# Performance work log

Hardware: AMD Instinct MI355X
Metric: run time of the kernel (lower is better)

The kernel has to match this reference:

```python
import jax, jax.numpy as jnp
import numpy as np

N_NODES = 50000
N_EDGES = 800000
HIDDEN = 128
OUT = 128


def setup_inputs() -> dict:
    key = jax.random.key(0)
    k1, k2, k3, k4, k5, k6 = jax.random.split(key, 6)
    h = jax.random.normal(k1, (N_NODES, HIDDEN), dtype=jnp.float32)
    src = jax.random.randint(k2, (N_EDGES,), 0, N_NODES, dtype=jnp.int64)
    dst = jax.random.randint(k3, (N_EDGES,), 0, N_NODES, dtype=jnp.int64)
    scale = 1.0 / np.sqrt(HIDDEN)
    W_edge = jax.random.normal(k4, (OUT, HIDDEN), dtype=jnp.float32) * scale
    W_self = jax.random.normal(k5, (OUT, HIDDEN), dtype=jnp.float32) * scale
    b_self = jax.random.normal(k6, (OUT,), dtype=jnp.float32) * scale
    return {"h": h, "src": src, "dst": dst, "W_edge": W_edge, "W_self": W_self, "b_self": b_self}


def reference(h, src, dst, W_edge, W_self, b_self):
    n = h.shape[0]
    # edge_transform(src_features): same linear on every edge -> transform nodes once, then gather
    msg_node = h @ W_edge.T                       # [N, OUT]
    msg = msg_node[src]                           # [E, OUT] gather
    sums = jax.ops.segment_sum(msg, dst, num_segments=n)  # [N, OUT] scatter-add
    deg = jax.ops.segment_sum(jnp.ones((dst.shape[0],), dtype=h.dtype), dst, num_segments=n)
    h1 = sums / jnp.maximum(deg, 1.0)[:, None]    # mean; zero in-degree -> 0 (DGL semantics)
    out = jax.nn.relu(h @ W_self.T + b_self + h1)
    return out
```

## Files before the change

kernel.cpp:

```cpp
#include <hip/hip_runtime.h>

#define N_HID 128
#define CAP   32
#define OVF_CAP 8192
#define NSLICE 8
#define PBLK   256

typedef short bf16x8 __attribute__((ext_vector_type(8)));
typedef float f32x4  __attribute__((ext_vector_type(4)));

static __device__ __forceinline__ unsigned short f2bf(float f)
{
    unsigned int u = __float_as_uint(f);
    u = (u + 0x7fffu + ((u >> 16) & 1u)) >> 16;
    return (unsigned short)u;
}
static __device__ __forceinline__ unsigned int pack2(float a, float b)
{
    return (unsigned int)f2bf(a) | ((unsigned int)f2bf(b) << 16);
}
static __device__ __forceinline__ float lo_f(unsigned int x)
{
    return __uint_as_float(x << 16);
}
static __device__ __forceinline__ float hi_f(unsigned int x)
{
    return __uint_as_float(x & 0xffff0000u);
}
static __device__ __forceinline__ int slice_of(int d, float sln)
{
    int sl = (int)((float)d * sln);
    return sl > NSLICE - 1 ? NSLICE - 1 : sl;
}

__global__ __launch_bounds__(256) void count_fragw_cast(
    const int* __restrict__ dst, int* __restrict__ blockCnt,
    int* __restrict__ cnt, int* __restrict__ ovfn, int E, int n, float sln,
    const float* __restrict__ We, const float* __restrict__ Ws,
    unsigned short* __restrict__ Be, unsigned short* __restrict__ Bs,
    const float* __restrict__ h, unsigned short* __restrict__ hbf, int total,
    unsigned int* __restrict__ bucket32, unsigned int sent2)
{
    int t = threadIdx.x, b = blockIdx.x;

    if (b >= PBLK + 16) {
        int idx = (b - PBLK - 16) * 2048 + t * 8;
        if (idx + 8 <= total) {
            float4 v0 = *(const float4*)&h[idx];
            float4 v1 = *(const float4*)&h[idx + 4];
            uint4 pk;
            pk.x = pack2(v0.x, v0.y);
            pk.y = pack2(v0.z, v0.w);
            pk.z = pack2(v1.x, v1.y);
            pk.w = pack2(v1.z, v1.w);
            *(uint4*)&hbf[idx] = pk;
        } else if (idx + 8 <= total + N_HID) {
            uint4 z = {0u, 0u, 0u, 0u};
            *(uint4*)&hbf[idx] = z;
        }
        return;
    }

    if (b >= PBLK) {
        int bb = b - PBLK;
        const float* srcw = (bb < 8) ? We : Ws;
        unsigned short* dstF = (bb < 8) ? Be : Bs;
        int rt = bb & 7;
        int kc = t >> 6, l = t & 63, m = l & 15, q = l >> 4;
        const float* p = &srcw[(size_t)(rt * 16 + m) * N_HID + kc * 32 + q * 8];
        float4 v0 = *(const float4*)p;
        float4 v1 = *(const float4*)(p + 4);
        uint4 pk;
        pk.x = pack2(v0.x, v0.y);
        pk.y = pack2(v0.z, v0.w);
        pk.z = pack2(v1.x, v1.y);
        pk.w = pack2(v1.z, v1.w);
        *(uint4*)&dstF[(size_t)rt * 2048 + kc * 512 + l * 8] = pk;
        return;
    }

    for (int i = b * 256 + t; i < n; i += PBLK * 256) cnt[i] = 0;
    {
        const int nb32 = n * (CAP / 2);
        for (int i = b * 256 + t; i < nb32; i += PBLK * 256) bucket32[i] = sent2;
    }
    if (b == 0 && t == 0) *ovfn = 0;

    int c[NSLICE];
#pragma unroll
    for (int s = 0; s < NSLICE; ++s) c[s] = 0;

    for (int e = b * 256 + t; e < E; e += PBLK * 256) {
        int sl = slice_of(dst[e], sln);
#pragma unroll
        for (int s = 0; s < NSLICE; ++s) c[s] += (sl == s);
    }

    __shared__ int red[NSLICE * 4];
    int lane = t & 63, wid = t >> 6;
#pragma unroll
    for (int s = 0; s < NSLICE; ++s) {
        int v = c[s];
#pragma unroll
        for (int off = 32; off; off >>= 1) v += __shfl_down(v, off);
        if (lane == 0) red[s * 4 + wid] = v;
    }
    __syncthreads();
    if (t < NSLICE)
        blockCnt[t * PBLK + b] = red[t*4+0] + red[t*4+1] + red[t*4+2] + red[t*4+3];
}

__global__ __launch_bounds__(256) void part_scan(
    const int* __restrict__ blockCnt, int* __restrict__ blockBase,
    int* __restrict__ sbase, int E)
{
    __shared__ int wsm[4];
    int t = threadIdx.x, lane = t & 63, wid = t >> 6;
    int v[8]; int s = 0;
#pragma unroll
    for (int i = 0; i < 8; ++i) { v[i] = blockCnt[t * 8 + i]; s += v[i]; }
    int val = s;
#pragma unroll
    for (int off = 1; off < 64; off <<= 1) {
        int y = __shfl_up(val, off);
        if (lane >= off) val += y;
    }
    if (lane == 63) wsm[wid] = val;
    __syncthreads();
    if (t == 0) { int a = 0; for (int w = 0; w < 4; ++w) { int tmp = wsm[w]; wsm[w] = a; a += tmp; } }
    __syncthreads();
    int excl = wsm[wid] + val - s;
#pragma unroll
    for (int i = 0; i < 8; ++i) { int tv = v[i]; blockBase[t * 8 + i] = excl; excl += tv; }
    __syncthreads();
    if (t < NSLICE) sbase[t] = blockBase[t * PBLK];
    if (t == 0)     sbase[NSLICE] = E;
}

__global__ __launch_bounds__(256) void part_scatter(
    const int* __restrict__ src, const int* __restrict__ dst,
    const int* __restrict__ blockBase, unsigned int* __restrict__ part,
    int E, int n, float sln)
{
    __shared__ int cur[NSLICE];
    int t = threadIdx.x, b = blockIdx.x;
    if (t < NSLICE) cur[t] = blockBase[t * PBLK + b];
    __syncthreads();
    for (int e = b * 256 + t; e < E; e += PBLK * 256) {
        int d = dst[e], s = src[e];
        int sl  = slice_of(d, sln);
        int pos = atomicAdd(&cur[sl], 1);
        part[pos] = ((unsigned int)d << 16) | (unsigned int)s;
    }
}

__global__ __launch_bounds__(256) void bucket_scatter2(
    const unsigned int* __restrict__ part,
    const int* __restrict__ sbase,
    int* __restrict__ cnt,
    unsigned short* __restrict__ bucket,
    int* __restrict__ ovfn,
    long long* __restrict__ ovf)
{
    const int slice = blockIdx.x & 7;
    const int g     = blockIdx.x >> 3;
    const int nG    = (int)(gridDim.x >> 3);
    const int lo    = sbase[slice];
    const int hi    = sbase[slice + 1];
    const int m     = hi - lo;

    const int chunk = (m + nG - 1) / nG;
    const int e0 = lo + g * chunk;
    int e1 = e0 + chunk; if (e1 > hi) e1 = hi;

    for (int e = e0 + (int)threadIdx.x; e < e1; e += 256) {
        unsigned int pk = part[e];
        int d = (int)(pk >> 16);
        int s = (int)(pk & 0xffffu);
        int c = atomicAdd(&cnt[d], 1);
        if (c < CAP) {
            bucket[(size_t)d * CAP + c] = (unsigned short)s;
        } else {
            int o = atomicAdd(ovfn, 1);
            if (o < OVF_CAP) ovf[o] = ((long long)d << 32) | (unsigned int)s;
        }
    }
}

__global__ __launch_bounds__(512) void gather_gemm(
    const int* __restrict__ cnt,
    const unsigned short* __restrict__ bucket,
    const int* __restrict__ ovfn,
    const long long* __restrict__ ovf,
    const unsigned short* __restrict__ hbf,
    const unsigned short* __restrict__ Be,
    const unsigned short* __restrict__ Bsf,
    const float* __restrict__ bias,
    float* __restrict__ out,
    int n, int nrt)
{
    __shared__ __align__(16) unsigned int wl[16 * 68];

    const int t    = threadIdx.x;
    const int wid  = t >> 6;
    const int lane = t & 63;
    const int q    = lane >> 4;
    const int s    = lane & 15;
    const int slice = blockIdx.x & 7;
    const int g     = blockIdx.x >> 3;
    const int tLo = (int)(((long long)slice * nrt) >> 3);
    const int tHi = (int)(((long long)(slice + 1) * nrt) >> 3);
    const int tile = tLo + g;
    if (tile >= tHi) return;

    const uint4* h4 = (const uint4*)hbf;

#pragma unroll
    for (int k = 0; k < 2; ++k) {
        const int mm   = wid * 2 + k;
        const int node = tile * 16 + mm;
        const unsigned short* bk = &bucket[(size_t)node * CAP];
        float a0=0.f,a1=0.f,a2=0.f,a3=0.f,a4=0.f,a5=0.f,a6=0.f,a7=0.f;
        int deg = node < n ? cnt[node] : 0;

        {
            uint4 vr[4];
#pragma unroll
            for (int i = 0; i < 4; ++i) {
                int r = bk[i * 4 + q];
                vr[i] = h4[(size_t)r * 16 + s];
            }
#pragma unroll
            for (int i = 0; i < 4; ++i) {
                a0 += lo_f(vr[i].x); a1 += hi_f(vr[i].x);
                a2 += lo_f(vr[i].y); a3 += hi_f(vr[i].y);
                a4 += lo_f(vr[i].z); a5 += hi_f(vr[i].z);
                a6 += lo_f(vr[i].w); a7 += hi_f(vr[i].w);
            }
        }
        if (deg > 16) {
            uint4 vr[4];
#pragma unroll
            for (int i = 0; i < 4; ++i) {
                int r = bk[16 + i * 4 + q];
                vr[i] = h4[(size_t)r * 16 + s];
            }
#pragma unroll
            for (int i = 0; i < 4; ++i) {
                a0 += lo_f(vr[i].x); a1 += hi_f(vr[i].x);
                a2 += lo_f(vr[i].y); a3 += hi_f(vr[i].y);
                a4 += lo_f(vr[i].z); a5 += hi_f(vr[i].z);
                a6 += lo_f(vr[i].w); a7 += hi_f(vr[i].w);
            }
        }

        if (deg > CAP) {
            int no = *ovfn; if (no > OVF_CAP) no = OVF_CAP;
            unsigned int qm = (q == 0) ? 0xffffffffu : 0u;
            for (int o = 0; o < no; ++o) {
                long long pk = ovf[o];
                if ((int)(pk >> 32) == node) {
                    uint4 v = h4[(size_t)(unsigned int)pk * 16 + s];
                    unsigned int x;
                    x = v.x & qm; a0 += lo_f(x); a1 += hi_f(x);
                    x = v.y & qm; a2 += lo_f(x); a3 += hi_f(x);
                    x = v.z & qm; a4 += lo_f(x); a5 += hi_f(x);
                    x = v.w & qm; a6 += lo_f(x); a7 += hi_f(x);
                }
            }
        }

#pragma unroll
        for (int off = 16; off <= 32; off <<= 1) {
            a0 += __shfl_xor(a0, off); a1 += __shfl_xor(a1, off);
            a2 += __shfl_xor(a2, off); a3 += __shfl_xor(a3, off);
            a4 += __shfl_xor(a4, off); a5 += __shfl_xor(a5, off);
            a6 += __shfl_xor(a6, off); a7 += __shfl_xor(a7, off);
        }

        float sc = deg > 0 ? 1.0f / (float)deg : 0.f;
        if (q == 0) {
            uint4 pk;
            pk.x = pack2(a0 * sc, a1 * sc);
            pk.y = pack2(a2 * sc, a3 * sc);
            pk.z = pack2(a4 * sc, a5 * sc);
            pk.w = pack2(a6 * sc, a7 * sc);
            *(uint4*)&wl[mm * 68 + 4 * s] = pk;
        }
    }
    __syncthreads();

    const int rr = lane & 15, qq = lane >> 4;
    const int row0 = tile * 16;

    bf16x8 ah[4], ag[4];
#pragma unroll
    for (int kc = 0; kc < 4; ++kc) {
        int gr = row0 + rr; if (gr > n - 1) gr = n - 1;
        ah[kc] = *(const bf16x8*)&hbf[(size_t)gr * N_HID + kc * 32 + qq * 8];
        ag[kc] = *(const bf16x8*)&wl[rr * 68 + kc * 16 + qq * 4];
    }

    const int colb = lane & 15;
    const int rq   = (lane >> 4) * 4;

    {
        int ct = wid;
        const bf16x8* BpS = (const bf16x8*)(Bsf + (size_t)ct * 2048);
        const bf16x8* BpE = (const bf16x8*)(Be  + (size_t)ct * 2048);
        f32x4 acc = {0.f, 0.f, 0.f, 0.f};
        acc = __builtin_amdgcn_mfma_f32_16x16x32_bf16(ah[0], BpS[lane],       acc, 0, 0, 0);
        acc = __builtin_amdgcn_mfma_f32_16x16x32_bf16(ah[1], BpS[64 + lane],  acc, 0, 0, 0);
        acc = __builtin_amdgcn_mfma_f32_16x16x32_bf16(ah[2], BpS[128 + lane], acc, 0, 0, 0);
        acc = __builtin_amdgcn_mfma_f32_16x16x32_bf16(ah[3], BpS[192 + lane], acc, 0, 0, 0);
        acc = __builtin_amdgcn_mfma_f32_16x16x32_bf16(ag[0], BpE[lane],       acc, 0, 0, 0);
        acc = __builtin_amdgcn_mfma_f32_16x16x32_bf16(ag[1], BpE[64 + lane],  acc, 0, 0, 0);
        acc = __builtin_amdgcn_mfma_f32_16x16x32_bf16(ag[2], BpE[128 + lane], acc, 0, 0, 0);
        acc = __builtin_amdgcn_mfma_f32_16x16x32_bf16(ag[3], BpE[192 + lane], acc, 0, 0, 0);

        int col = ct * 16 + colb;
        float bv = bias[col];
#pragma unroll
        for (int r = 0; r < 4; ++r) {
            int row = row0 + rq + r;
            if (row < n) out[(size_t)row * N_HID + col] = fmaxf(acc[r] + bv, 0.f);
        }
    }
}

extern "C" void kernel_launch(void* const* d_in, const int* in_sizes, int n_in,
                              void* d_out, int out_size, void* d_ws, size_t ws_size,
                              hipStream_t stream)
{
    const float* h   = (const float*)d_in[0];
    const int*   src = (const int*)d_in[1];
    const int*   dst = (const int*)d_in[2];
    const float* We  = (const float*)d_in[3];
    const float* Ws  = (const float*)d_in[4];
    const float* bs  = (const float*)d_in[5];
    float*       out = (float*)d_out;

    const int n   = in_sizes[0] / N_HID;
    const int E   = in_sizes[1];
    const int nrt = (n + 15) / 16;
    const float sln = (float)NSLICE / (float)n;
    const int total = n * N_HID;

    unsigned short* hbf  = (unsigned short*)d_ws;
    unsigned short* bucket = hbf + (size_t)(n + 1) * N_HID;
    unsigned short* Be  = bucket + (size_t)n * CAP;
    unsigned short* Bs  = Be + 8 * 2048;
    int*  cnt  = (int*)(Bs + 8 * 2048);
    int*  ovfn = cnt + n;
    long long* ovf = (long long*)(ovfn + 8);
    int*  blockCnt  = (int*)(ovf + OVF_CAP);
    int*  blockBase = blockCnt + PBLK * NSLICE;
    int*  sbase     = blockBase + PBLK * NSLICE;
    unsigned int* part = (unsigned int*)(sbase + 16);

    const unsigned int sent2 = (unsigned int)n | ((unsigned int)n << 16);
    const int castBlocks = (total + N_HID + 2047) / 2048;

    const int maxTilesPerSlice = (nrt + NSLICE - 1) / NSLICE;
    const int ggGrid = NSLICE * maxTilesPerSlice;

    count_fragw_cast<<<PBLK + 16 + castBlocks, 256, 0, stream>>>(
        dst, blockCnt, cnt, ovfn, E, n, sln, We, Ws, Be, Bs, h, hbf, total,
        (unsigned int*)bucket, sent2);
    part_scan<<<1, 256, 0, stream>>>(blockCnt, blockBase, sbase, E);
    part_scatter<<<PBLK, 256, 0, stream>>>(src, dst, blockBase, part, E, n, sln);
    bucket_scatter2<<<1024, 256, 0, stream>>>(part, sbase, cnt, bucket, ovfn, ovf);
    gather_gemm<<<ggGrid, 512, 0, stream>>>(cnt, bucket, ovfn, ovf,
                                            hbf, Be, Bs, bs, out, n, nrt);
}
```

Measured before the change: 179.8 us.

## Rework gather to one full-row dword per lane with 4-wave blocks

The gather phase changes from four edges per wave instruction (uint4 per lane, 16-lane groups) to one edge per wave instruction, where each of the 64 lanes loads one dword of the bf16 row. This removes the cross-lane shuffle reduction and the masked overflow path. Blocks shrink from 8 to 4 waves, and each wave now handles 4 nodes in the gather and 2 column tiles in the MFMA stage. The trade is more load instructions per node, each with a scalar index read, in exchange for fewer reductions and a smaller block.

```diff
diff --git a/kernel.cpp b/kernel.cpp
--- a/kernel.cpp
+++ b/kernel.cpp
@@ -187,7 +187,7 @@
     }
 }
 
-__global__ __launch_bounds__(512) void gather_gemm(
+__global__ __launch_bounds__(256) void gather_gemm(
     const int* __restrict__ cnt,
     const unsigned short* __restrict__ bucket,
     const int* __restrict__ ovfn,
@@ -202,10 +202,8 @@
     __shared__ __align__(16) unsigned int wl[16 * 68];
 
     const int t    = threadIdx.x;
-    const int wid  = t >> 6;
     const int lane = t & 63;
-    const int q    = lane >> 4;
-    const int s    = lane & 15;
+    const int widu = __builtin_amdgcn_readfirstlane(t >> 6);
     const int slice = blockIdx.x & 7;
     const int g     = blockIdx.x >> 3;
     const int tLo = (int)(((long long)slice * nrt) >> 3);
@@ -213,80 +211,57 @@
     const int tile = tLo + g;
     if (tile >= tHi) return;
 
-    const uint4* h4 = (const uint4*)hbf;
-
-#pragma unroll
-    for (int k = 0; k < 2; ++k) {
-        const int mm   = wid * 2 + k;
+    const unsigned int* h32 = (const unsigned int*)hbf;
+
+#pragma unroll
+    for (int k = 0; k < 4; ++k) {
+        const int mm   = widu * 4 + k;
         const int node = tile * 16 + mm;
-        const unsigned short* bk = &bucket[(size_t)node * CAP];
-        float a0=0.f,a1=0.f,a2=0.f,a3=0.f,a4=0.f,a5=0.f,a6=0.f,a7=0.f;
-        int deg = node < n ? cnt[node] : 0;
-
-        {
-            uint4 vr[4];
-#pragma unroll
-            for (int i = 0; i < 4; ++i) {
-                int r = bk[i * 4 + q];
-                vr[i] = h4[(size_t)r * 16 + s];
+        float ax = 0.f, ay = 0.f;
+        int deg = 0;
+        if (node < n) {
+            deg = cnt[node];
+            const unsigned short* bk = &bucket[(size_t)node * CAP];
+
+            {
+                unsigned int v[16];
+#pragma unroll
+                for (int i = 0; i < 16; ++i) {
+                    const unsigned int r = bk[i];
+                    v[i] = h32[(size_t)r * 64 + lane];
+                }
+#pragma unroll
+                for (int i = 0; i < 16; ++i) {
+                    ax += lo_f(v[i]); ay += hi_f(v[i]);
+                }
             }
-#pragma unroll
-            for (int i = 0; i < 4; ++i) {
-                a0 += lo_f(vr[i].x); a1 += hi_f(vr[i].x);
-                a2 += lo_f(vr[i].y); a3 += hi_f(vr[i].y);
-                a4 += lo_f(vr[i].z); a5 += hi_f(vr[i].z);
-                a6 += lo_f(vr[i].w); a7 += hi_f(vr[i].w);
+            if (deg > 16) {
+                unsigned int v[16];
+#pragma unroll
+                for (int i = 0; i < 16; ++i) {
+                    const unsigned int r = bk[16 + i];
+                    v[i] = h32[(size_t)r * 64 + lane];
+                }
+#pragma unroll
+                for (int i = 0; i < 16; ++i) {
+                    ax += lo_f(v[i]); ay += hi_f(v[i]);
+                }
+            }
+
+            if (deg > CAP) {
+                int no = *ovfn; if (no > OVF_CAP) no = OVF_CAP;
+                for (int o = 0; o < no; ++o) {
+                    long long pk = ovf[o];
+                    if ((int)(pk >> 32) == node) {
+                        unsigned int x = h32[(size_t)(unsigned int)pk * 64 + lane];
+                        ax += lo_f(x); ay += hi_f(x);
+                    }
+                }
             }
         }
-        if (deg > 16) {
-            uint4 vr[4];
-#pragma unroll
-            for (int i = 0; i < 4; ++i) {
-                int r = bk[16 + i * 4 + q];
-                vr[i] = h4[(size_t)r * 16 + s];
-            }
-#pragma unroll
-            for (int i = 0; i < 4; ++i) {
-                a0 += lo_f(vr[i].x); a1 += hi_f(vr[i].x);
-                a2 += lo_f(vr[i].y); a3 += hi_f(vr[i].y);
-                a4 += lo_f(vr[i].z); a5 += hi_f(vr[i].z);
-                a6 += lo_f(vr[i].w); a7 += hi_f(vr[i].w);
-            }
-        }
-
-        if (deg > CAP) {
-            int no = *ovfn; if (no > OVF_CAP) no = OVF_CAP;
-            unsigned int qm = (q == 0) ? 0xffffffffu : 0u;
-            for (int o = 0; o < no; ++o) {
-                long long pk = ovf[o];
-                if ((int)(pk >> 32) == node) {
-                    uint4 v = h4[(size_t)(unsigned int)pk * 16 + s];
-                    unsigned int x;
-                    x = v.x & qm; a0 += lo_f(x); a1 += hi_f(x);
-                    x = v.y & qm; a2 += lo_f(x); a3 += hi_f(x);
-                    x = v.z & qm; a4 += lo_f(x); a5 += hi_f(x);
-                    x = v.w & qm; a6 += lo_f(x); a7 += hi_f(x);
-                }
-            }
-        }
-
-#pragma unroll
-        for (int off = 16; off <= 32; off <<= 1) {
-            a0 += __shfl_xor(a0, off); a1 += __shfl_xor(a1, off);
-            a2 += __shfl_xor(a2, off); a3 += __shfl_xor(a3, off);
-            a4 += __shfl_xor(a4, off); a5 += __shfl_xor(a5, off);
-            a6 += __shfl_xor(a6, off); a7 += __shfl_xor(a7, off);
-        }
 
         float sc = deg > 0 ? 1.0f / (float)deg : 0.f;
-        if (q == 0) {
-            uint4 pk;
-            pk.x = pack2(a0 * sc, a1 * sc);
-            pk.y = pack2(a2 * sc, a3 * sc);
-            pk.z = pack2(a4 * sc, a5 * sc);
-            pk.w = pack2(a6 * sc, a7 * sc);
-            *(uint4*)&wl[mm * 68 + 4 * s] = pk;
-        }
+        wl[mm * 68 + lane] = pack2(ax * sc, ay * sc);
     }
     __syncthreads();
 
@@ -304,8 +279,9 @@
     const int colb = lane & 15;
     const int rq   = (lane >> 4) * 4;
 
-    {
-        int ct = wid;
+#pragma unroll
+    for (int cti = 0; cti < 2; ++cti) {
+        int ct = widu * 2 + cti;
         const bf16x8* BpS = (const bf16x8*)(Bsf + (size_t)ct * 2048);
         const bf16x8* BpE = (const bf16x8*)(Be  + (size_t)ct * 2048);
         f32x4 acc = {0.f, 0.f, 0.f, 0.f};
@@ -370,6 +346,6 @@
     part_scan<<<1, 256, 0, stream>>>(blockCnt, blockBase, sbase, E);
     part_scatter<<<PBLK, 256, 0, stream>>>(src, dst, blockBase, part, E, n, sln);
     bucket_scatter2<<<1024, 256, 0, stream>>>(part, sbase, cnt, bucket, ovfn, ovf);
-    gather_gemm<<<ggGrid, 512, 0, stream>>>(cnt, bucket, ovfn, ovf,
+    gather_gemm<<<ggGrid, 256, 0, stream>>>(cnt, bucket, ovfn, ovf,
                                             hbf, Be, Bs, bs, out, n, nrt);
 }
```

Measured after the change: 173.7 us. 1.03x faster.
